# Kernel tuning notes

Hardware: AMD Instinct MI355X
Metric: run time of the kernel (lower is better)

The kernel has to match this reference:

```python
import jax, jax.numpy as jnp
import numpy as np

N_PTS = 262144
RES = 256
PLANE_DIM = 32
VIEW_FREQ = 4


def view_embed(d):
    # NeRF positional embedding with include_input, log-spaced freqs 2^0..2^(F-1)
    # d: [M, 3] -> [M, 3*(1+2F)] = [M, 27] for F=4
    freqs = (2.0 ** jnp.arange(VIEW_FREQ)).astype(d.dtype)  # [F]
    ang = d[:, None, :] * freqs[None, :, None]              # [M, F, 3]
    return jnp.concatenate(
        [d, jnp.sin(ang).reshape(d.shape[0], -1), jnp.cos(ang).reshape(d.shape[0], -1)], axis=1)


def bilinear_sample(plane, gx, gy):
    # plane: [C, H, W]; gx, gy: [N] grid coords in [-1, 1] (x indexes W, y indexes H).
    # Matches torch grid_sample(mode='bilinear', align_corners=True, padding_mode='zeros').
    C, H, W = plane.shape
    px = (gx + 1.0) * 0.5 * (W - 1)
    py = (gy + 1.0) * 0.5 * (H - 1)
    x0 = jnp.floor(px)
    y0 = jnp.floor(py)
    fx = px - x0
    fy = py - y0
    x0i = x0.astype(jnp.int32)
    y0i = y0.astype(jnp.int32)

    def gather(xi, yi):
        valid = ((xi >= 0) & (xi <= W - 1) & (yi >= 0) & (yi <= H - 1)).astype(plane.dtype)
        xc = jnp.clip(xi, 0, W - 1)
        yc = jnp.clip(yi, 0, H - 1)
        return plane[:, yc, xc] * valid[None, :]  # [C, N]

    return (gather(x0i,     y0i)     * ((1 - fx) * (1 - fy))[None, :]
          + gather(x0i + 1, y0i)     * (fx       * (1 - fy))[None, :]
          + gather(x0i,     y0i + 1) * ((1 - fx) * fy)[None, :]
          + gather(x0i + 1, y0i + 1) * (fx       * fy)[None, :])


def mlp3(x, W1, b1, W2, b2, W3, b3):
    h = jax.nn.relu(x @ W1 + b1)
    h = jax.nn.relu(h @ W2 + b2)
    return h @ W3 + b3  # last_op=None


def setup_inputs() -> dict:
    key = jax.random.key(0)
    ks = jax.random.split(key, 12)
    B = 1
    query_pts = jax.random.uniform(ks[0], (B, 3, N_PTS), jnp.float32, -1.0, 1.0)
    vd = jax.random.normal(ks[1], (B, 3, N_PTS), jnp.float32)
    query_viewdirs = vd / (jnp.linalg.norm(vd, axis=1, keepdims=True) + 1e-8)
    triplanes = jax.random.normal(ks[2], (B, 3 * PLANE_DIM, RES, RES), jnp.float32) * 0.1

    def lin(k, fi, fo):
        return jax.random.normal(k, (fi, fo), jnp.float32) / np.sqrt(fi).astype(np.float32)

    return {
        'query_pts': query_pts, 'query_viewdirs': query_viewdirs, 'triplanes': triplanes,
        'dW1': lin(ks[3], 32, 128),  'dB1': jnp.zeros((128,), jnp.float32),
        'dW2': lin(ks[4], 128, 128), 'dB2': jnp.zeros((128,), jnp.float32),
        'dW3': lin(ks[5], 128, 1),   'dB3': jnp.zeros((1,), jnp.float32),
        'cW1': lin(ks[6], 59, 128),  'cB1': jnp.zeros((128,), jnp.float32),
        'cW2': lin(ks[7], 128, 128), 'cB2': jnp.zeros((128,), jnp.float32),
        'cW3': lin(ks[8], 128, 3),   'cB3': jnp.zeros((3,), jnp.float32),
    }


def reference(query_pts, query_viewdirs, triplanes,
              dW1, dB1, dW2, dB2, dW3, dB3,
              cW1, cB1, cW2, cB2, cW3, cB3):
    B, _, N = query_pts.shape
    plane_dim = triplanes.shape[1] // 3
    plane_x = triplanes[:, 0 * plane_dim:1 * plane_dim]
    plane_y = triplanes[:, 1 * plane_dim:2 * plane_dim]
    plane_z = triplanes[:, 2 * plane_dim:3 * plane_dim]
    # bbox = unit cube -> u,v,w are the raw coordinates
    u, v, w = query_pts[:, 0], query_pts[:, 1], query_pts[:, 2]  # each [B, N]
    samp = jax.vmap(bilinear_sample)
    # grid (x, y) ordering: vw -> x=v, y=w ; uw -> x=u, y=w ; uv -> x=u, y=v
    feature = samp(plane_x, v, w) + samp(plane_y, u, w) + samp(plane_z, u, v)  # [B, C, N]
    feat_flat = feature.transpose(0, 2, 1).reshape(B * N, plane_dim)           # [(B N), C]

    density = mlp3(feat_flat, dW1, dB1, dW2, dB2, dW3, dB3)                    # [(B N), 1]
    vd_flat = query_viewdirs.transpose(0, 2, 1).reshape(B * N, 3)
    color_in = jnp.concatenate([feat_flat, view_embed(vd_flat)], axis=1)        # [(B N), 59]
    color = mlp3(color_in, cW1, cB1, cW2, cB2, cW3, cB3)                       # [(B N), 3]

    density = density.reshape(B, N, 1).transpose(0, 2, 1)  # [B, 1, N]
    color = color.reshape(B, N, 3).transpose(0, 2, 1)      # [B, 3, N]
    return jnp.concatenate([density, color], axis=1)        # [B, 4, N]
```

## Files before the change

kernel.cpp:

```cpp
#include <hip/hip_runtime.h>

#define NPTS 262144
#define RES  256
#define PD   32

typedef unsigned short u16;
typedef unsigned int   u32;

typedef __bf16 bf16x8 __attribute__((ext_vector_type(8)));
typedef float  f32x4  __attribute__((ext_vector_type(4)));
typedef u32    u32x2  __attribute__((ext_vector_type(2)));

__device__ __forceinline__ u16 f2bf(float f) {
    return __builtin_bit_cast(u16, (__bf16)f);
}
__device__ __forceinline__ float bf2f(u32 u) {
    return __builtin_bit_cast(float, (u32)(u << 16));
}
__device__ __forceinline__ u32 pk2(float a, float b) {
    return (u32)f2bf(a) | ((u32)f2bf(b) << 16);
}

__global__ void k_transpose_planes(const float* __restrict__ tp, u16* __restrict__ dst) {
    const int b  = blockIdx.x;
    const int pl = b >> 8, y = b & 255;
    const int x  = threadIdx.x;
    const float* src = tp + ((size_t)pl * PD * RES + y) * RES + x;
    u32 w[16];
#pragma unroll
    for (int c = 0; c < 16; ++c) {
        const float v0 = src[(size_t)(2 * c)     * (RES * RES)];
        const float v1 = src[(size_t)(2 * c + 1) * (RES * RES)];
        w[c] = (u32)f2bf(v0) | ((u32)f2bf(v1) << 16);
    }
    uint4* d = (uint4*)(dst + (size_t)((pl * RES + y) * RES + x) * PD);
    d[0] = make_uint4(w[0],  w[1],  w[2],  w[3]);
    d[1] = make_uint4(w[4],  w[5],  w[6],  w[7]);
    d[2] = make_uint4(w[8],  w[9],  w[10], w[11]);
    d[3] = make_uint4(w[12], w[13], w[14], w[15]);
}

__global__ void k_prep_weights(const float* __restrict__ dW1, const float* __restrict__ dW2,
                               const float* __restrict__ cW1, const float* __restrict__ cW2,
                               const float* __restrict__ cW3,
                               u16* __restrict__ w1d, u16* __restrict__ w1c,
                               u16* __restrict__ w2d, u16* __restrict__ w2c,
                               float* __restrict__ w3ct) {
    const int tid = blockIdx.x * 256 + threadIdx.x;
    if (tid < 128 * 32) { const int n = tid >> 5, k = tid & 31; w1d[tid] = f2bf(dW1[k * 128 + n]); }
    if (tid < 128 * 64) { const int n = tid >> 6, k = tid & 63; w1c[tid] = f2bf(k < 59 ? cW1[k * 128 + n] : 0.f); }
    if (tid < 3 * 128) { w3ct[tid] = cW3[(tid & 127) * 3 + (tid >> 7)]; }
    { const int n = tid >> 7, k = tid & 127;
      w2d[tid] = f2bf(dW2[k * 128 + n]);
      w2c[tid] = f2bf(cW2[k * 128 + n]); }
}

__global__ __launch_bounds__(256) void k_fused(
    const float* __restrict__ pts, const float* __restrict__ vds,
    const u16* __restrict__ planes,
    const u16* __restrict__ gW1d, const u16* __restrict__ gW1c,
    const u16* __restrict__ gW2d, const u16* __restrict__ gW2c,
    const float* __restrict__ gB1d, const float* __restrict__ gB2d,
    const float* __restrict__ gW3d, const float* __restrict__ gB3d,
    const float* __restrict__ gB1c, const float* __restrict__ gB2c,
    const float* __restrict__ gW3ct, const float* __restrict__ gB3c,
    float* __restrict__ out) {
    __shared__ __align__(16) u16 sX[64 * 64];
    __shared__ __align__(16) u16 sH[64 * 128];
    __shared__ float sAcc[4 * 64];

    const int t    = threadIdx.x;
    const int lane = t & 63;
    const int wc   = t >> 6;
    const int l15  = lane & 15;
    const int l4   = lane >> 4;
    const int kb   = l4 * 16;
    const int pbase = blockIdx.x * 64;
    const f32x4 FZ = {0.f, 0.f, 0.f, 0.f};

    sAcc[t] = 0.f;

    bf16x8 b1d[2];
#pragma unroll
    for (int nl = 0; nl < 2; ++nl) {
        const int n = wc * 32 + nl * 16 + l15;
        b1d[nl] = *(const bf16x8*)(gW1d + n * 32 + l4 * 8);
    }

    {
        const int p = t >> 2, q = t & 3;
        const int pg = pbase + p;
        const int sw = (p & 7) << 4;
        const float pu = pts[pg], pv = pts[NPTS + pg], pw = pts[2 * NPTS + pg];

        uint4 tv[12];
        float wts[12];

#pragma unroll
        for (int pl = 0; pl < 3; ++pl) {
            const float gx = (pl == 0) ? pv : pu;
            const float gy = (pl == 2) ? pv : pw;
            const float px = (gx + 1.f) * 127.5f;
            const float py = (gy + 1.f) * 127.5f;
            const float x0 = floorf(px), y0 = floorf(py);
            const float fx = px - x0, fy = py - y0;
            const int ix = (int)x0, iy = (int)y0;
            const u16* pb = planes + (size_t)pl * (RES * RES * PD) + q * 8;
#pragma unroll
            for (int dy = 0; dy < 2; ++dy) {
#pragma unroll
                for (int dx = 0; dx < 2; ++dx) {
                    const int i = pl * 4 + dy * 2 + dx;
                    const int xi = ix + dx, yi = iy + dy;
                    float wt = (dx ? fx : 1.f - fx) * (dy ? fy : 1.f - fy);
                    if (xi < 0 || xi > RES - 1 || yi < 0 || yi > RES - 1) wt = 0.f;
                    const int xc = xi < 0 ? 0 : (xi > RES - 1 ? RES - 1 : xi);
                    const int yc = yi < 0 ? 0 : (yi > RES - 1 ? RES - 1 : yi);
                    wts[i] = wt;
                    tv[i] = *(const uint4*)(pb + ((size_t)(yc * RES + xc) << 5));
                }
            }
        }

        float facc[8] = {0.f, 0.f, 0.f, 0.f, 0.f, 0.f, 0.f, 0.f};
#pragma unroll
        for (int i = 0; i < 12; ++i) {
            const float wt = wts[i];
            const uint4 v = tv[i];
            facc[0] += wt * bf2f(v.x & 0xffffu);
            facc[1] += wt * bf2f(v.x >> 16);
            facc[2] += wt * bf2f(v.y & 0xffffu);
            facc[3] += wt * bf2f(v.y >> 16);
            facc[4] += wt * bf2f(v.z & 0xffffu);
            facc[5] += wt * bf2f(v.z >> 16);
            facc[6] += wt * bf2f(v.w & 0xffffu);
            facc[7] += wt * bf2f(v.w >> 16);
        }
        {
            u32 wp[4];
#pragma unroll
            for (int i = 0; i < 4; ++i) wp[i] = pk2(facc[2 * i], facc[2 * i + 1]);
            *(uint4*)((char*)sX + p * 128 + ((q * 16) ^ sw)) =
                make_uint4(wp[0], wp[1], wp[2], wp[3]);
        }

        if (q == 1 || q == 2) {
            const float d0 = vds[pg], d1 = vds[NPTS + pg], d2 = vds[2 * NPTS + pg];
            float e[16];
            if (q == 1) {
                e[0] = d0; e[1] = d1; e[2] = d2;
#pragma unroll
                for (int f = 0; f < 4; ++f) {
                    const float fr = (float)(1 << f);
                    e[3 + f * 3 + 0] = __sinf(d0 * fr);
                    e[3 + f * 3 + 1] = __sinf(d1 * fr);
                    e[3 + f * 3 + 2] = __sinf(d2 * fr);
                }
                e[15] = __cosf(d0);
            } else {
                e[0] = __cosf(d1); e[1] = __cosf(d2);
#pragma unroll
                for (int f = 1; f < 4; ++f) {
                    const float fr = (float)(1 << f);
                    e[2 + (f - 1) * 3 + 0] = __cosf(d0 * fr);
                    e[2 + (f - 1) * 3 + 1] = __cosf(d1 * fr);
                    e[2 + (f - 1) * 3 + 2] = __cosf(d2 * fr);
                }
#pragma unroll
                for (int i = 11; i < 16; ++i) e[i] = 0.f;
            }
            const int base = 64 + (q - 1) * 32;
#pragma unroll
            for (int g = 0; g < 2; ++g) {
                const u32 a0 = pk2(e[8 * g + 0], e[8 * g + 1]);
                const u32 a1 = pk2(e[8 * g + 2], e[8 * g + 3]);
                const u32 a2 = pk2(e[8 * g + 4], e[8 * g + 5]);
                const u32 a3 = pk2(e[8 * g + 6], e[8 * g + 7]);
                *(uint4*)((char*)sX + p * 128 + ((base + g * 16) ^ sw)) =
                    make_uint4(a0, a1, a2, a3);
            }
        }
    }

    bf16x8 b2dp[4];
#pragma unroll
    for (int nl = 0; nl < 2; ++nl)
#pragma unroll
        for (int kk = 0; kk < 2; ++kk) {
            const int n = wc * 32 + nl * 16 + l15;
            b2dp[nl * 2 + kk] = *(const bf16x8*)(gW2d + n * 128 + kk * 32 + l4 * 8);
        }
    __syncthreads();

    bf16x8 b1cp[4];

    {
        f32x4 acc[4][2];
        bf16x8 a[4];
#pragma unroll
        for (int mt = 0; mt < 4; ++mt) {
            const int m = mt * 16 + l15;
            a[mt] = *(const bf16x8*)((const char*)sX + m * 128 + (kb ^ ((m & 7) << 4)));
#pragma unroll
            for (int nl = 0; nl < 2; ++nl) acc[mt][nl] = FZ;
        }
#pragma unroll
        for (int nl = 0; nl < 2; ++nl)
#pragma unroll
            for (int mt = 0; mt < 4; ++mt)
                acc[mt][nl] = __builtin_amdgcn_mfma_f32_16x16x32_bf16(b1d[nl], a[mt], acc[mt][nl], 0, 0, 0);

#pragma unroll
        for (int nl = 0; nl < 2; ++nl)
#pragma unroll
            for (int kk = 0; kk < 2; ++kk) {
                const int n = wc * 32 + nl * 16 + l15;
                b1cp[nl * 2 + kk] = *(const bf16x8*)(gW1c + n * 64 + kk * 32 + l4 * 8);
            }

#pragma unroll
        for (int nl = 0; nl < 2; ++nl) {
            const int n0 = wc * 32 + nl * 16 + l4 * 4;
            const f32x4 bv = *(const f32x4*)(gB1d + n0);
#pragma unroll
            for (int mt = 0; mt < 4; ++mt) {
                const int m = mt * 16 + l15;
                const float h0 = fmaxf(acc[mt][nl][0] + bv[0], 0.f);
                const float h1 = fmaxf(acc[mt][nl][1] + bv[1], 0.f);
                const float h2 = fmaxf(acc[mt][nl][2] + bv[2], 0.f);
                const float h3 = fmaxf(acc[mt][nl][3] + bv[3], 0.f);
                *(u32x2*)((char*)sH + m * 256 + ((n0 * 2) ^ ((m & 7) << 4))) =
                    u32x2{pk2(h0, h1), pk2(h2, h3)};
            }
        }
    }
    __syncthreads();

    bf16x8 b2cp[4];

    {
        f32x4 bv[2], wv[2];
#pragma unroll
        for (int nl = 0; nl < 2; ++nl) {
            const int n0 = wc * 32 + nl * 16 + l4 * 4;
            bv[nl] = *(const f32x4*)(gB2d + n0);
            wv[nl] = *(const f32x4*)(gW3d + n0);
        }

        f32x4 acc[4][2];
#pragma unroll
        for (int mt = 0; mt < 4; ++mt)
#pragma unroll
            for (int nl = 0; nl < 2; ++nl) acc[mt][nl] = FZ;
#pragma unroll
        for (int kk = 0; kk < 4; ++kk) {
            bf16x8 a[4];
#pragma unroll
            for (int mt = 0; mt < 4; ++mt) {
                const int m = mt * 16 + l15;
                a[mt] = *(const bf16x8*)((const char*)sH + m * 256 + ((kk * 64 + kb) ^ ((m & 7) << 4)));
            }
#pragma unroll
            for (int nl = 0; nl < 2; ++nl) {
                const int n = wc * 32 + nl * 16 + l15;
                const bf16x8 b = (kk < 2) ? b2dp[nl * 2 + kk]
                                          : *(const bf16x8*)(gW2d + n * 128 + kk * 32 + l4 * 8);
#pragma unroll
                for (int mt = 0; mt < 4; ++mt)
                    acc[mt][nl] = __builtin_amdgcn_mfma_f32_16x16x32_bf16(b, a[mt], acc[mt][nl], 0, 0, 0);
            }
        }

#pragma unroll
        for (int nl = 0; nl < 2; ++nl)
#pragma unroll
            for (int kk = 0; kk < 2; ++kk) {
                const int n = wc * 32 + nl * 16 + l15;
                b2cp[nl * 2 + kk] = *(const bf16x8*)(gW2c + n * 128 + kk * 32 + l4 * 8);
            }

#pragma unroll
        for (int mt = 0; mt < 4; ++mt) {
            float s = 0.f;
#pragma unroll
            for (int nl = 0; nl < 2; ++nl)
#pragma unroll
                for (int r = 0; r < 4; ++r) {
                    const float h = fmaxf(acc[mt][nl][r] + bv[nl][r], 0.f);
                    s += h * wv[nl][r];
                }
            s += __shfl_xor(s, 16);
            s += __shfl_xor(s, 32);
            if (l4 == 0)
                atomicAdd(&sAcc[0 * 64 + mt * 16 + l15], s);
        }
    }
    __syncthreads();

    {
        f32x4 acc[4][2];
#pragma unroll
        for (int mt = 0; mt < 4; ++mt)
#pragma unroll
            for (int nl = 0; nl < 2; ++nl) acc[mt][nl] = FZ;
#pragma unroll
        for (int kk = 0; kk < 2; ++kk) {
            bf16x8 a[4];
#pragma unroll
            for (int mt = 0; mt < 4; ++mt) {
                const int m = mt * 16 + l15;
                a[mt] = *(const bf16x8*)((const char*)sX + m * 128 + ((kk * 64 + kb) ^ ((m & 7) << 4)));
            }
#pragma unroll
            for (int nl = 0; nl < 2; ++nl)
#pragma unroll
                for (int mt = 0; mt < 4; ++mt)
                    acc[mt][nl] = __builtin_amdgcn_mfma_f32_16x16x32_bf16(b1cp[nl * 2 + kk], a[mt], acc[mt][nl], 0, 0, 0);
        }
#pragma unroll
        for (int nl = 0; nl < 2; ++nl) {
            const int n0 = wc * 32 + nl * 16 + l4 * 4;
            const f32x4 bv = *(const f32x4*)(gB1c + n0);
#pragma unroll
            for (int mt = 0; mt < 4; ++mt) {
                const int m = mt * 16 + l15;
                const float h0 = fmaxf(acc[mt][nl][0] + bv[0], 0.f);
                const float h1 = fmaxf(acc[mt][nl][1] + bv[1], 0.f);
                const float h2 = fmaxf(acc[mt][nl][2] + bv[2], 0.f);
                const float h3 = fmaxf(acc[mt][nl][3] + bv[3], 0.f);
                *(u32x2*)((char*)sH + m * 256 + ((n0 * 2) ^ ((m & 7) << 4))) =
                    u32x2{pk2(h0, h1), pk2(h2, h3)};
            }
        }
    }
    __syncthreads();

    {
        f32x4 bv[2], w0v[2], w1v[2], w2v[2];
#pragma unroll
        for (int nl = 0; nl < 2; ++nl) {
            const int n0 = wc * 32 + nl * 16 + l4 * 4;
            bv[nl]  = *(const f32x4*)(gB2c + n0);
            w0v[nl] = *(const f32x4*)(gW3ct + 0 * 128 + n0);
            w1v[nl] = *(const f32x4*)(gW3ct + 1 * 128 + n0);
            w2v[nl] = *(const f32x4*)(gW3ct + 2 * 128 + n0);
        }

        f32x4 acc[4][2];
#pragma unroll
        for (int mt = 0; mt < 4; ++mt)
#pragma unroll
            for (int nl = 0; nl < 2; ++nl) acc[mt][nl] = FZ;
#pragma unroll
        for (int kk = 0; kk < 4; ++kk) {
            bf16x8 a[4];
#pragma unroll
            for (int mt = 0; mt < 4; ++mt) {
                const int m = mt * 16 + l15;
                a[mt] = *(const bf16x8*)((const char*)sH + m * 256 + ((kk * 64 + kb) ^ ((m & 7) << 4)));
            }
#pragma unroll
            for (int nl = 0; nl < 2; ++nl) {
                const int n = wc * 32 + nl * 16 + l15;
                const bf16x8 b = (kk < 2) ? b2cp[nl * 2 + kk]
                                          : *(const bf16x8*)(gW2c + n * 128 + kk * 32 + l4 * 8);
#pragma unroll
                for (int mt = 0; mt < 4; ++mt)
                    acc[mt][nl] = __builtin_amdgcn_mfma_f32_16x16x32_bf16(b, a[mt], acc[mt][nl], 0, 0, 0);
            }
        }

#pragma unroll
        for (int mt = 0; mt < 4; ++mt) {
            float s0 = 0.f, s1 = 0.f, s2 = 0.f;
#pragma unroll
            for (int nl = 0; nl < 2; ++nl)
#pragma unroll
                for (int r = 0; r < 4; ++r) {
                    const float h = fmaxf(acc[mt][nl][r] + bv[nl][r], 0.f);
                    s0 += h * w0v[nl][r];
                    s1 += h * w1v[nl][r];
                    s2 += h * w2v[nl][r];
                }
            s0 += __shfl_xor(s0, 16); s0 += __shfl_xor(s0, 32);
            s1 += __shfl_xor(s1, 16); s1 += __shfl_xor(s1, 32);
            s2 += __shfl_xor(s2, 16); s2 += __shfl_xor(s2, 32);
            if (l4 == 0) {
                atomicAdd(&sAcc[1 * 64 + mt * 16 + l15], s0);
                atomicAdd(&sAcc[2 * 64 + mt * 16 + l15], s1);
                atomicAdd(&sAcc[3 * 64 + mt * 16 + l15], s2);
            }
        }
    }
    __syncthreads();

    {
        const int ch = t >> 6, row = t & 63;
        const float bias = (ch == 0) ? gB3d[0] : gB3c[ch - 1];
        out[(size_t)ch * NPTS + pbase + row] = sAcc[ch * 64 + row] + bias;
    }
}

extern "C" void kernel_launch(void* const* d_in, const int* in_sizes, int n_in,
                              void* d_out, int out_size, void* d_ws, size_t ws_size,
                              hipStream_t stream) {
    (void)in_sizes; (void)n_in; (void)out_size; (void)ws_size;
    const float* pts = (const float*)d_in[0];
    const float* vds = (const float*)d_in[1];
    const float* tp  = (const float*)d_in[2];
    const float* dW1 = (const float*)d_in[3];
    const float* dB1 = (const float*)d_in[4];
    const float* dW2 = (const float*)d_in[5];
    const float* dB2 = (const float*)d_in[6];
    const float* dW3 = (const float*)d_in[7];
    const float* dB3 = (const float*)d_in[8];
    const float* cW1 = (const float*)d_in[9];
    const float* cB1 = (const float*)d_in[10];
    const float* cW2 = (const float*)d_in[11];
    const float* cB2 = (const float*)d_in[12];
    const float* cW3 = (const float*)d_in[13];
    const float* cB3 = (const float*)d_in[14];
    float* out = (float*)d_out;

    u16* planes_t = (u16*)d_ws;
    u16* w1d = planes_t + (size_t)3 * RES * RES * PD;
    u16* w1c = w1d + 128 * 32;
    u16* w2d = w1c + 128 * 64;
    u16* w2c = w2d + 128 * 128;
    float* w3ct = (float*)(w2c + 128 * 128);

    k_transpose_planes<<<3 * RES, 256, 0, stream>>>(tp, planes_t);
    k_prep_weights<<<64, 256, 0, stream>>>(dW1, dW2, cW1, cW2, cW3,
                                           w1d, w1c, w2d, w2c, w3ct);
    k_fused<<<NPTS / 64, 256, 0, stream>>>(pts, vds, planes_t,
                                           w1d, w1c, w2d, w2c,
                                           dB1, dB2, dW3, dB3,
                                           cB1, cB2, w3ct, cB3,
                                           out);
}
```

Before: 88.91 us.

## Process two point tiles per block and prefetch second tile's plane gathers

Each block now handles 128 points as two 64-point tiles. During the first tile's MLP stages it issues the triplane gather loads for the second tile into registers, so gather latency overlaps with MFMA work. This halves the grid size and adds twelve uint4 prefetch registers per thread, which raises register pressure and may reduce occupancy.

```diff
diff --git a/kernel.cpp b/kernel.cpp
--- a/kernel.cpp
+++ b/kernel.cpp
@@ -67,7 +67,7 @@
     float* __restrict__ out) {
     __shared__ __align__(16) u16 sX[64 * 64];
     __shared__ __align__(16) u16 sH[64 * 128];
-    __shared__ float sAcc[4 * 64];
+    __shared__ float sAcc[2][4 * 64];
 
     const int t    = threadIdx.x;
     const int lane = t & 63;
@@ -75,10 +75,10 @@
     const int l15  = lane & 15;
     const int l4   = lane >> 4;
     const int kb   = l4 * 16;
-    const int pbase = blockIdx.x * 64;
     const f32x4 FZ = {0.f, 0.f, 0.f, 0.f};
 
-    sAcc[t] = 0.f;
+    sAcc[0][t] = 0.f;
+    sAcc[1][t] = 0.f;
 
     bf16x8 b1d[2];
 #pragma unroll
@@ -87,317 +87,355 @@
         b1d[nl] = *(const bf16x8*)(gW1d + n * 32 + l4 * 8);
     }
 
-    {
-        const int p = t >> 2, q = t & 3;
-        const int pg = pbase + p;
-        const int sw = (p & 7) << 4;
-        const float pu = pts[pg], pv = pts[NPTS + pg], pw = pts[2 * NPTS + pg];
-
-        uint4 tv[12];
-        float wts[12];
-
-#pragma unroll
-        for (int pl = 0; pl < 3; ++pl) {
-            const float gx = (pl == 0) ? pv : pu;
-            const float gy = (pl == 2) ? pv : pw;
-            const float px = (gx + 1.f) * 127.5f;
-            const float py = (gy + 1.f) * 127.5f;
-            const float x0 = floorf(px), y0 = floorf(py);
-            const float fx = px - x0, fy = py - y0;
-            const int ix = (int)x0, iy = (int)y0;
-            const u16* pb = planes + (size_t)pl * (RES * RES * PD) + q * 8;
-#pragma unroll
-            for (int dy = 0; dy < 2; ++dy) {
-#pragma unroll
-                for (int dx = 0; dx < 2; ++dx) {
-                    const int i = pl * 4 + dy * 2 + dx;
-                    const int xi = ix + dx, yi = iy + dy;
-                    float wt = (dx ? fx : 1.f - fx) * (dy ? fy : 1.f - fy);
-                    if (xi < 0 || xi > RES - 1 || yi < 0 || yi > RES - 1) wt = 0.f;
-                    const int xc = xi < 0 ? 0 : (xi > RES - 1 ? RES - 1 : xi);
-                    const int yc = yi < 0 ? 0 : (yi > RES - 1 ? RES - 1 : yi);
-                    wts[i] = wt;
-                    tv[i] = *(const uint4*)(pb + ((size_t)(yc * RES + xc) << 5));
-                }
-            }
-        }
-
-        float facc[8] = {0.f, 0.f, 0.f, 0.f, 0.f, 0.f, 0.f, 0.f};
-#pragma unroll
-        for (int i = 0; i < 12; ++i) {
-            const float wt = wts[i];
-            const uint4 v = tv[i];
-            facc[0] += wt * bf2f(v.x & 0xffffu);
-            facc[1] += wt * bf2f(v.x >> 16);
-            facc[2] += wt * bf2f(v.y & 0xffffu);
-            facc[3] += wt * bf2f(v.y >> 16);
-            facc[4] += wt * bf2f(v.z & 0xffffu);
-            facc[5] += wt * bf2f(v.z >> 16);
-            facc[6] += wt * bf2f(v.w & 0xffffu);
-            facc[7] += wt * bf2f(v.w >> 16);
-        }
-        {
-            u32 wp[4];
-#pragma unroll
-            for (int i = 0; i < 4; ++i) wp[i] = pk2(facc[2 * i], facc[2 * i + 1]);
-            *(uint4*)((char*)sX + p * 128 + ((q * 16) ^ sw)) =
-                make_uint4(wp[0], wp[1], wp[2], wp[3]);
-        }
-
-        if (q == 1 || q == 2) {
-            const float d0 = vds[pg], d1 = vds[NPTS + pg], d2 = vds[2 * NPTS + pg];
-            float e[16];
-            if (q == 1) {
-                e[0] = d0; e[1] = d1; e[2] = d2;
-#pragma unroll
-                for (int f = 0; f < 4; ++f) {
-                    const float fr = (float)(1 << f);
-                    e[3 + f * 3 + 0] = __sinf(d0 * fr);
-                    e[3 + f * 3 + 1] = __sinf(d1 * fr);
-                    e[3 + f * 3 + 2] = __sinf(d2 * fr);
-                }
-                e[15] = __cosf(d0);
-            } else {
-                e[0] = __cosf(d1); e[1] = __cosf(d2);
-#pragma unroll
-                for (int f = 1; f < 4; ++f) {
-                    const float fr = (float)(1 << f);
-                    e[2 + (f - 1) * 3 + 0] = __cosf(d0 * fr);
-                    e[2 + (f - 1) * 3 + 1] = __cosf(d1 * fr);
-                    e[2 + (f - 1) * 3 + 2] = __cosf(d2 * fr);
-                }
-#pragma unroll
-                for (int i = 11; i < 16; ++i) e[i] = 0.f;
-            }
-            const int base = 64 + (q - 1) * 32;
-#pragma unroll
-            for (int g = 0; g < 2; ++g) {
-                const u32 a0 = pk2(e[8 * g + 0], e[8 * g + 1]);
-                const u32 a1 = pk2(e[8 * g + 2], e[8 * g + 3]);
-                const u32 a2 = pk2(e[8 * g + 4], e[8 * g + 5]);
-                const u32 a3 = pk2(e[8 * g + 6], e[8 * g + 7]);
-                *(uint4*)((char*)sX + p * 128 + ((base + g * 16) ^ sw)) =
-                    make_uint4(a0, a1, a2, a3);
-            }
-        }
-    }
-
-    bf16x8 b2dp[4];
-#pragma unroll
-    for (int nl = 0; nl < 2; ++nl)
-#pragma unroll
-        for (int kk = 0; kk < 2; ++kk) {
-            const int n = wc * 32 + nl * 16 + l15;
-            b2dp[nl * 2 + kk] = *(const bf16x8*)(gW2d + n * 128 + kk * 32 + l4 * 8);
-        }
-    __syncthreads();
-
-    bf16x8 b1cp[4];
-
-    {
-        f32x4 acc[4][2];
-        bf16x8 a[4];
-#pragma unroll
-        for (int mt = 0; mt < 4; ++mt) {
-            const int m = mt * 16 + l15;
-            a[mt] = *(const bf16x8*)((const char*)sX + m * 128 + (kb ^ ((m & 7) << 4)));
-#pragma unroll
-            for (int nl = 0; nl < 2; ++nl) acc[mt][nl] = FZ;
-        }
-#pragma unroll
-        for (int nl = 0; nl < 2; ++nl)
-#pragma unroll
-            for (int mt = 0; mt < 4; ++mt)
-                acc[mt][nl] = __builtin_amdgcn_mfma_f32_16x16x32_bf16(b1d[nl], a[mt], acc[mt][nl], 0, 0, 0);
-
+    uint4 tvp[12];
+
+#pragma unroll
+    for (int tile = 0; tile < 2; ++tile) {
+        const int pbase = blockIdx.x * 128 + tile * 64;
+        float* sAccT = sAcc[tile];
+
+        {
+            const int p = t >> 2, q = t & 3;
+            const int pg = pbase + p;
+            const int sw = (p & 7) << 4;
+            const float pu = pts[pg], pv = pts[NPTS + pg], pw = pts[2 * NPTS + pg];
+
+            uint4 tv[12];
+            float wts[12];
+
+#pragma unroll
+            for (int pl = 0; pl < 3; ++pl) {
+                const float gx = (pl == 0) ? pv : pu;
+                const float gy = (pl == 2) ? pv : pw;
+                const float px = (gx + 1.f) * 127.5f;
+                const float py = (gy + 1.f) * 127.5f;
+                const float x0 = floorf(px), y0 = floorf(py);
+                const float fx = px - x0, fy = py - y0;
+                const int ix = (int)x0, iy = (int)y0;
+                const u16* pb = planes + (size_t)pl * (RES * RES * PD) + q * 8;
+#pragma unroll
+                for (int dy = 0; dy < 2; ++dy) {
+#pragma unroll
+                    for (int dx = 0; dx < 2; ++dx) {
+                        const int i = pl * 4 + dy * 2 + dx;
+                        const int xi = ix + dx, yi = iy + dy;
+                        float wt = (dx ? fx : 1.f - fx) * (dy ? fy : 1.f - fy);
+                        if (xi < 0 || xi > RES - 1 || yi < 0 || yi > RES - 1) wt = 0.f;
+                        const int xc = xi < 0 ? 0 : (xi > RES - 1 ? RES - 1 : xi);
+                        const int yc = yi < 0 ? 0 : (yi > RES - 1 ? RES - 1 : yi);
+                        wts[i] = wt;
+                        if (tile == 0)
+                            tv[i] = *(const uint4*)(pb + ((size_t)(yc * RES + xc) << 5));
+                        else
+                            tv[i] = tvp[i];
+                    }
+                }
+            }
+
+            float facc[8] = {0.f, 0.f, 0.f, 0.f, 0.f, 0.f, 0.f, 0.f};
+#pragma unroll
+            for (int i = 0; i < 12; ++i) {
+                const float wt = wts[i];
+                const uint4 v = tv[i];
+                facc[0] += wt * bf2f(v.x & 0xffffu);
+                facc[1] += wt * bf2f(v.x >> 16);
+                facc[2] += wt * bf2f(v.y & 0xffffu);
+                facc[3] += wt * bf2f(v.y >> 16);
+                facc[4] += wt * bf2f(v.z & 0xffffu);
+                facc[5] += wt * bf2f(v.z >> 16);
+                facc[6] += wt * bf2f(v.w & 0xffffu);
+                facc[7] += wt * bf2f(v.w >> 16);
+            }
+            {
+                u32 wp[4];
+#pragma unroll
+                for (int i = 0; i < 4; ++i) wp[i] = pk2(facc[2 * i], facc[2 * i + 1]);
+                *(uint4*)((char*)sX + p * 128 + ((q * 16) ^ sw)) =
+                    make_uint4(wp[0], wp[1], wp[2], wp[3]);
+            }
+
+            if (q == 1 || q == 2) {
+                const float d0 = vds[pg], d1 = vds[NPTS + pg], d2 = vds[2 * NPTS + pg];
+                float e[16];
+                if (q == 1) {
+                    e[0] = d0; e[1] = d1; e[2] = d2;
+#pragma unroll
+                    for (int f = 0; f < 4; ++f) {
+                        const float fr = (float)(1 << f);
+                        e[3 + f * 3 + 0] = __sinf(d0 * fr);
+                        e[3 + f * 3 + 1] = __sinf(d1 * fr);
+                        e[3 + f * 3 + 2] = __sinf(d2 * fr);
+                    }
+                    e[15] = __cosf(d0);
+                } else {
+                    e[0] = __cosf(d1); e[1] = __cosf(d2);
+#pragma unroll
+                    for (int f = 1; f < 4; ++f) {
+                        const float fr = (float)(1 << f);
+                        e[2 + (f - 1) * 3 + 0] = __cosf(d0 * fr);
+                        e[2 + (f - 1) * 3 + 1] = __cosf(d1 * fr);
+                        e[2 + (f - 1) * 3 + 2] = __cosf(d2 * fr);
+                    }
+#pragma unroll
+                    for (int i = 11; i < 16; ++i) e[i] = 0.f;
+                }
+                const int base = 64 + (q - 1) * 32;
+#pragma unroll
+                for (int g = 0; g < 2; ++g) {
+                    const u32 a0 = pk2(e[8 * g + 0], e[8 * g + 1]);
+                    const u32 a1 = pk2(e[8 * g + 2], e[8 * g + 3]);
+                    const u32 a2 = pk2(e[8 * g + 4], e[8 * g + 5]);
+                    const u32 a3 = pk2(e[8 * g + 6], e[8 * g + 7]);
+                    *(uint4*)((char*)sX + p * 128 + ((base + g * 16) ^ sw)) =
+                        make_uint4(a0, a1, a2, a3);
+                }
+            }
+        }
+
+        bf16x8 b2dp[4];
 #pragma unroll
         for (int nl = 0; nl < 2; ++nl)
 #pragma unroll
             for (int kk = 0; kk < 2; ++kk) {
                 const int n = wc * 32 + nl * 16 + l15;
-                b1cp[nl * 2 + kk] = *(const bf16x8*)(gW1c + n * 64 + kk * 32 + l4 * 8);
-            }
-
-#pragma unroll
-        for (int nl = 0; nl < 2; ++nl) {
-            const int n0 = wc * 32 + nl * 16 + l4 * 4;
-            const f32x4 bv = *(const f32x4*)(gB1d + n0);
+                b2dp[nl * 2 + kk] = *(const bf16x8*)(gW2d + n * 128 + kk * 32 + l4 * 8);
+            }
+        __syncthreads();
+
+        bf16x8 b1cp[4];
+
+        {
+            f32x4 acc[4][2];
+            bf16x8 a[4];
 #pragma unroll
             for (int mt = 0; mt < 4; ++mt) {
                 const int m = mt * 16 + l15;
-                const float h0 = fmaxf(acc[mt][nl][0] + bv[0], 0.f);
-                const float h1 = fmaxf(acc[mt][nl][1] + bv[1], 0.f);
-                const float h2 = fmaxf(acc[mt][nl][2] + bv[2], 0.f);
-                const float h3 = fmaxf(acc[mt][nl][3] + bv[3], 0.f);
-                *(u32x2*)((char*)sH + m * 256 + ((n0 * 2) ^ ((m & 7) << 4))) =
-                    u32x2{pk2(h0, h1), pk2(h2, h3)};
-            }
-        }
-    }
-    __syncthreads();
-
-    bf16x8 b2cp[4];
-
-    {
-        f32x4 bv[2], wv[2];
-#pragma unroll
-        for (int nl = 0; nl < 2; ++nl) {
-            const int n0 = wc * 32 + nl * 16 + l4 * 4;
-            bv[nl] = *(const f32x4*)(gB2d + n0);
-            wv[nl] = *(const f32x4*)(gW3d + n0);
-        }
-
-        f32x4 acc[4][2];
-#pragma unroll
-        for (int mt = 0; mt < 4; ++mt)
-#pragma unroll
-            for (int nl = 0; nl < 2; ++nl) acc[mt][nl] = FZ;
-#pragma unroll
-        for (int kk = 0; kk < 4; ++kk) {
-            bf16x8 a[4];
+                a[mt] = *(const bf16x8*)((const char*)sX + m * 128 + (kb ^ ((m & 7) << 4)));
+#pragma unroll
+                for (int nl = 0; nl < 2; ++nl) acc[mt][nl] = FZ;
+            }
+#pragma unroll
+            for (int nl = 0; nl < 2; ++nl)
+#pragma unroll
+                for (int mt = 0; mt < 4; ++mt)
+                    acc[mt][nl] = __builtin_amdgcn_mfma_f32_16x16x32_bf16(b1d[nl], a[mt], acc[mt][nl], 0, 0, 0);
+
+#pragma unroll
+            for (int nl = 0; nl < 2; ++nl)
+#pragma unroll
+                for (int kk = 0; kk < 2; ++kk) {
+                    const int n = wc * 32 + nl * 16 + l15;
+                    b1cp[nl * 2 + kk] = *(const bf16x8*)(gW1c + n * 64 + kk * 32 + l4 * 8);
+                }
+
+#pragma unroll
+            for (int nl = 0; nl < 2; ++nl) {
+                const int n0 = wc * 32 + nl * 16 + l4 * 4;
+                const f32x4 bv = *(const f32x4*)(gB1d + n0);
+#pragma unroll
+                for (int mt = 0; mt < 4; ++mt) {
+                    const int m = mt * 16 + l15;
+                    const float h0 = fmaxf(acc[mt][nl][0] + bv[0], 0.f);
+                    const float h1 = fmaxf(acc[mt][nl][1] + bv[1], 0.f);
+                    const float h2 = fmaxf(acc[mt][nl][2] + bv[2], 0.f);
+                    const float h3 = fmaxf(acc[mt][nl][3] + bv[3], 0.f);
+                    *(u32x2*)((char*)sH + m * 256 + ((n0 * 2) ^ ((m & 7) << 4))) =
+                        u32x2{pk2(h0, h1), pk2(h2, h3)};
+                }
+            }
+        }
+        __syncthreads();
+
+        bf16x8 b2cp[4];
+
+        {
+            f32x4 bv[2], wv[2];
+#pragma unroll
+            for (int nl = 0; nl < 2; ++nl) {
+                const int n0 = wc * 32 + nl * 16 + l4 * 4;
+                bv[nl] = *(const f32x4*)(gB2d + n0);
+                wv[nl] = *(const f32x4*)(gW3d + n0);
+            }
+
+            f32x4 acc[4][2];
+#pragma unroll
+            for (int mt = 0; mt < 4; ++mt)
+#pragma unroll
+                for (int nl = 0; nl < 2; ++nl) acc[mt][nl] = FZ;
+#pragma unroll
+            for (int kk = 0; kk < 4; ++kk) {
+                bf16x8 a[4];
+#pragma unroll
+                for (int mt = 0; mt < 4; ++mt) {
+                    const int m = mt * 16 + l15;
+                    a[mt] = *(const bf16x8*)((const char*)sH + m * 256 + ((kk * 64 + kb) ^ ((m & 7) << 4)));
+                }
+#pragma unroll
+                for (int nl = 0; nl < 2; ++nl) {
+                    const int n = wc * 32 + nl * 16 + l15;
+                    const bf16x8 b = (kk < 2) ? b2dp[nl * 2 + kk]
+                                              : *(const bf16x8*)(gW2d + n * 128 + kk * 32 + l4 * 8);
+#pragma unroll
+                    for (int mt = 0; mt < 4; ++mt)
+                        acc[mt][nl] = __builtin_amdgcn_mfma_f32_16x16x32_bf16(b, a[mt], acc[mt][nl], 0, 0, 0);
+                }
+            }
+
+#pragma unroll
+            for (int nl = 0; nl < 2; ++nl)
+#pragma unroll
+                for (int kk = 0; kk < 2; ++kk) {
+                    const int n = wc * 32 + nl * 16 + l15;
+                    b2cp[nl * 2 + kk] = *(const bf16x8*)(gW2c + n * 128 + kk * 32 + l4 * 8);
+                }
+
 #pragma unroll
             for (int mt = 0; mt < 4; ++mt) {
-                const int m = mt * 16 + l15;
-                a[mt] = *(const bf16x8*)((const char*)sH + m * 256 + ((kk * 64 + kb) ^ ((m & 7) << 4)));
+                float s = 0.f;
+#pragma unroll
+                for (int nl = 0; nl < 2; ++nl)
+#pragma unroll
+                    for (int r = 0; r < 4; ++r) {
+                        const float h = fmaxf(acc[mt][nl][r] + bv[nl][r], 0.f);
+                        s += h * wv[nl][r];
+                    }
+                s += __shfl_xor(s, 16);
+                s += __shfl_xor(s, 32);
+                if (l4 == 0)
+                    atomicAdd(&sAccT[0 * 64 + mt * 16 + l15], s);
+            }
+        }
+        __syncthreads();
+
+        {
+            if (tile == 0) {
+                const int p2 = t >> 2, q2 = t & 3;
+                const int pg2 = blockIdx.x * 128 + 64 + p2;
+                const float pu2 = pts[pg2], pv2 = pts[NPTS + pg2], pw2 = pts[2 * NPTS + pg2];
+#pragma unroll
+                for (int pl = 0; pl < 3; ++pl) {
+                    const float gx = (pl == 0) ? pv2 : pu2;
+                    const float gy = (pl == 2) ? pv2 : pw2;
+                    const float px = (gx + 1.f) * 127.5f;
+                    const float py = (gy + 1.f) * 127.5f;
+                    const float x0 = floorf(px), y0 = floorf(py);
+                    const int ix = (int)x0, iy = (int)y0;
+                    const u16* pb = planes + (size_t)pl * (RES * RES * PD) + q2 * 8;
+#pragma unroll
+                    for (int dy = 0; dy < 2; ++dy) {
+#pragma unroll
+                        for (int dx = 0; dx < 2; ++dx) {
+                            const int i = pl * 4 + dy * 2 + dx;
+                            const int xi = ix + dx, yi = iy + dy;
+                            const int xc = xi < 0 ? 0 : (xi > RES - 1 ? RES - 1 : xi);
+                            const int yc = yi < 0 ? 0 : (yi > RES - 1 ? RES - 1 : yi);
+                            tvp[i] = *(const uint4*)(pb + ((size_t)(yc * RES + xc) << 5));
+                        }
+                    }
+                }
+            }
+
+            f32x4 acc[4][2];
+#pragma unroll
+            for (int mt = 0; mt < 4; ++mt)
+#pragma unroll
+                for (int nl = 0; nl < 2; ++nl) acc[mt][nl] = FZ;
+#pragma unroll
+            for (int kk = 0; kk < 2; ++kk) {
+                bf16x8 a[4];
+#pragma unroll
+                for (int mt = 0; mt < 4; ++mt) {
+                    const int m = mt * 16 + l15;
+                    a[mt] = *(const bf16x8*)((const char*)sX + m * 128 + ((kk * 64 + kb) ^ ((m & 7) << 4)));
+                }
+#pragma unroll
+                for (int nl = 0; nl < 2; ++nl)
+#pragma unroll
+                    for (int mt = 0; mt < 4; ++mt)
+                        acc[mt][nl] = __builtin_amdgcn_mfma_f32_16x16x32_bf16(b1cp[nl * 2 + kk], a[mt], acc[mt][nl], 0, 0, 0);
             }
 #pragma unroll
             for (int nl = 0; nl < 2; ++nl) {
-                const int n = wc * 32 + nl * 16 + l15;
-                const bf16x8 b = (kk < 2) ? b2dp[nl * 2 + kk]
-                                          : *(const bf16x8*)(gW2d + n * 128 + kk * 32 + l4 * 8);
-#pragma unroll
-                for (int mt = 0; mt < 4; ++mt)
-                    acc[mt][nl] = __builtin_amdgcn_mfma_f32_16x16x32_bf16(b, a[mt], acc[mt][nl], 0, 0, 0);
-            }
-        }
-
-#pragma unroll
-        for (int nl = 0; nl < 2; ++nl)
-#pragma unroll
-            for (int kk = 0; kk < 2; ++kk) {
-                const int n = wc * 32 + nl * 16 + l15;
-                b2cp[nl * 2 + kk] = *(const bf16x8*)(gW2c + n * 128 + kk * 32 + l4 * 8);
-            }
-
-#pragma unroll
-        for (int mt = 0; mt < 4; ++mt) {
-            float s = 0.f;
-#pragma unroll
-            for (int nl = 0; nl < 2; ++nl)
-#pragma unroll
-                for (int r = 0; r < 4; ++r) {
-                    const float h = fmaxf(acc[mt][nl][r] + bv[nl][r], 0.f);
-                    s += h * wv[nl][r];
-                }
-            s += __shfl_xor(s, 16);
-            s += __shfl_xor(s, 32);
-            if (l4 == 0)
-                atomicAdd(&sAcc[0 * 64 + mt * 16 + l15], s);
-        }
-    }
-    __syncthreads();
-
-    {
-        f32x4 acc[4][2];
-#pragma unroll
-        for (int mt = 0; mt < 4; ++mt)
-#pragma unroll
-            for (int nl = 0; nl < 2; ++nl) acc[mt][nl] = FZ;
-#pragma unroll
-        for (int kk = 0; kk < 2; ++kk) {
-            bf16x8 a[4];
+                const int n0 = wc * 32 + nl * 16 + l4 * 4;
+                const f32x4 bv = *(const f32x4*)(gB1c + n0);
+#pragma unroll
+                for (int mt = 0; mt < 4; ++mt) {
+                    const int m = mt * 16 + l15;
+                    const float h0 = fmaxf(acc[mt][nl][0] + bv[0], 0.f);
+                    const float h1 = fmaxf(acc[mt][nl][1] + bv[1], 0.f);
+                    const float h2 = fmaxf(acc[mt][nl][2] + bv[2], 0.f);
+                    const float h3 = fmaxf(acc[mt][nl][3] + bv[3], 0.f);
+                    *(u32x2*)((char*)sH + m * 256 + ((n0 * 2) ^ ((m & 7) << 4))) =
+                        u32x2{pk2(h0, h1), pk2(h2, h3)};
+                }
+            }
+        }
+        __syncthreads();
+
+        {
+            f32x4 bv[2], w0v[2], w1v[2], w2v[2];
+#pragma unroll
+            for (int nl = 0; nl < 2; ++nl) {
+                const int n0 = wc * 32 + nl * 16 + l4 * 4;
+                bv[nl]  = *(const f32x4*)(gB2c + n0);
+                w0v[nl] = *(const f32x4*)(gW3ct + 0 * 128 + n0);
+                w1v[nl] = *(const f32x4*)(gW3ct + 1 * 128 + n0);
+                w2v[nl] = *(const f32x4*)(gW3ct + 2 * 128 + n0);
+            }
+
+            f32x4 acc[4][2];
+#pragma unroll
+            for (int mt = 0; mt < 4; ++mt)
+#pragma unroll
+                for (int nl = 0; nl < 2; ++nl) acc[mt][nl] = FZ;
+#pragma unroll
+            for (int kk = 0; kk < 4; ++kk) {
+                bf16x8 a[4];
+#pragma unroll
+                for (int mt = 0; mt < 4; ++mt) {
+                    const int m = mt * 16 + l15;
+                    a[mt] = *(const bf16x8*)((const char*)sH + m * 256 + ((kk * 64 + kb) ^ ((m & 7) << 4)));
+                }
+#pragma unroll
+                for (int nl = 0; nl < 2; ++nl) {
+                    const int n = wc * 32 + nl * 16 + l15;
+                    const bf16x8 b = (kk < 2) ? b2cp[nl * 2 + kk]
+                                              : *(const bf16x8*)(gW2c + n * 128 + kk * 32 + l4 * 8);
+#pragma unroll
+                    for (int mt = 0; mt < 4; ++mt)
+                        acc[mt][nl] = __builtin_amdgcn_mfma_f32_16x16x32_bf16(b, a[mt], acc[mt][nl], 0, 0, 0);
+                }
+            }
+
 #pragma unroll
             for (int mt = 0; mt < 4; ++mt) {
-                const int m = mt * 16 + l15;
-                a[mt] = *(const bf16x8*)((const char*)sX + m * 128 + ((kk * 64 + kb) ^ ((m & 7) << 4)));
-            }
-#pragma unroll
-            for (int nl = 0; nl < 2; ++nl)
-#pragma unroll
-                for (int mt = 0; mt < 4; ++mt)
-                    acc[mt][nl] = __builtin_amdgcn_mfma_f32_16x16x32_bf16(b1cp[nl * 2 + kk], a[mt], acc[mt][nl], 0, 0, 0);
-        }
-#pragma unroll
-        for (int nl = 0; nl < 2; ++nl) {
-            const int n0 = wc * 32 + nl * 16 + l4 * 4;
-            const f32x4 bv = *(const f32x4*)(gB1c + n0);
-#pragma unroll
-            for (int mt = 0; mt < 4; ++mt) {
-                const int m = mt * 16 + l15;
-                const float h0 = fmaxf(acc[mt][nl][0] + bv[0], 0.f);
-                const float h1 = fmaxf(acc[mt][nl][1] + bv[1], 0.f);
-                const float h2 = fmaxf(acc[mt][nl][2] + bv[2], 0.f);
-                const float h3 = fmaxf(acc[mt][nl][3] + bv[3], 0.f);
-                *(u32x2*)((char*)sH + m * 256 + ((n0 * 2) ^ ((m & 7) << 4))) =
-                    u32x2{pk2(h0, h1), pk2(h2, h3)};
-            }
-        }
-    }
-    __syncthreads();
-
-    {
-        f32x4 bv[2], w0v[2], w1v[2], w2v[2];
-#pragma unroll
-        for (int nl = 0; nl < 2; ++nl) {
-            const int n0 = wc * 32 + nl * 16 + l4 * 4;
-            bv[nl]  = *(const f32x4*)(gB2c + n0);
-            w0v[nl] = *(const f32x4*)(gW3ct + 0 * 128 + n0);
-            w1v[nl] = *(const f32x4*)(gW3ct + 1 * 128 + n0);
-            w2v[nl] = *(const f32x4*)(gW3ct + 2 * 128 + n0);
-        }
-
-        f32x4 acc[4][2];
-#pragma unroll
-        for (int mt = 0; mt < 4; ++mt)
-#pragma unroll
-            for (int nl = 0; nl < 2; ++nl) acc[mt][nl] = FZ;
-#pragma unroll
-        for (int kk = 0; kk < 4; ++kk) {
-            bf16x8 a[4];
-#pragma unroll
-            for (int mt = 0; mt < 4; ++mt) {
-                const int m = mt * 16 + l15;
-                a[mt] = *(const bf16x8*)((const char*)sH + m * 256 + ((kk * 64 + kb) ^ ((m & 7) << 4)));
-            }
-#pragma unroll
-            for (int nl = 0; nl < 2; ++nl) {
-                const int n = wc * 32 + nl * 16 + l15;
-                const bf16x8 b = (kk < 2) ? b2cp[nl * 2 + kk]
-                                          : *(const bf16x8*)(gW2c + n * 128 + kk * 32 + l4 * 8);
-#pragma unroll
-                for (int mt = 0; mt < 4; ++mt)
-                    acc[mt][nl] = __builtin_amdgcn_mfma_f32_16x16x32_bf16(b, a[mt], acc[mt][nl], 0, 0, 0);
-            }
-        }
-
-#pragma unroll
-        for (int mt = 0; mt < 4; ++mt) {
-            float s0 = 0.f, s1 = 0.f, s2 = 0.f;
-#pragma unroll
-            for (int nl = 0; nl < 2; ++nl)
-#pragma unroll
-                for (int r = 0; r < 4; ++r) {
-                    const float h = fmaxf(acc[mt][nl][r] + bv[nl][r], 0.f);
-                    s0 += h * w0v[nl][r];
-                    s1 += h * w1v[nl][r];
-                    s2 += h * w2v[nl][r];
-                }
-            s0 += __shfl_xor(s0, 16); s0 += __shfl_xor(s0, 32);
-            s1 += __shfl_xor(s1, 16); s1 += __shfl_xor(s1, 32);
-            s2 += __shfl_xor(s2, 16); s2 += __shfl_xor(s2, 32);
-            if (l4 == 0) {
-                atomicAdd(&sAcc[1 * 64 + mt * 16 + l15], s0);
-                atomicAdd(&sAcc[2 * 64 + mt * 16 + l15], s1);
-                atomicAdd(&sAcc[3 * 64 + mt * 16 + l15], s2);
-            }
-        }
-    }
-    __syncthreads();
-
-    {
-        const int ch = t >> 6, row = t & 63;
-        const float bias = (ch == 0) ? gB3d[0] : gB3c[ch - 1];
-        out[(size_t)ch * NPTS + pbase + row] = sAcc[ch * 64 + row] + bias;
+                float s0 = 0.f, s1 = 0.f, s2 = 0.f;
+#pragma unroll
+                for (int nl = 0; nl < 2; ++nl)
+#pragma unroll
+                    for (int r = 0; r < 4; ++r) {
+                        const float h = fmaxf(acc[mt][nl][r] + bv[nl][r], 0.f);
+                        s0 += h * w0v[nl][r];
+                        s1 += h * w1v[nl][r];
+                        s2 += h * w2v[nl][r];
+                    }
+                s0 += __shfl_xor(s0, 16); s0 += __shfl_xor(s0, 32);
+                s1 += __shfl_xor(s1, 16); s1 += __shfl_xor(s1, 32);
+                s2 += __shfl_xor(s2, 16); s2 += __shfl_xor(s2, 32);
+                if (l4 == 0) {
+                    atomicAdd(&sAccT[1 * 64 + mt * 16 + l15], s0);
+                    atomicAdd(&sAccT[2 * 64 + mt * 16 + l15], s1);
+                    atomicAdd(&sAccT[3 * 64 + mt * 16 + l15], s2);
+                }
+            }
+        }
+        __syncthreads();
+
+        {
+            const int ch = t >> 6, row = t & 63;
+            const float bias = (ch == 0) ? gB3d[0] : gB3c[ch - 1];
+            out[(size_t)ch * NPTS + pbase + row] = sAccT[ch * 64 + row] + bias;
+        }
     }
 }
 
@@ -432,9 +470,9 @@
     k_transpose_planes<<<3 * RES, 256, 0, stream>>>(tp, planes_t);
     k_prep_weights<<<64, 256, 0, stream>>>(dW1, dW2, cW1, cW2, cW3,
                                            w1d, w1c, w2d, w2c, w3ct);
-    k_fused<<<NPTS / 64, 256, 0, stream>>>(pts, vds, planes_t,
-                                           w1d, w1c, w2d, w2c,
-                                           dB1, dB2, dW3, dB3,
-                                           cB1, cB2, w3ct, cB3,
-                                           out);
-}
+    k_fused<<<NPTS / 128, 256, 0, stream>>>(pts, vds, planes_t,
+                                            w1d, w1c, w2d, w2c,
+                                            dB1, dB2, dW3, dB3,
+                                            cB1, cB2, w3ct, cB3,
+                                            out);
+}
```

Measured after the change: 108.9 us. +22.5%, slower.
